# Optimization experiments

Measured on AMD Instinct MI355X. Metric: run time of the kernel, lower is better.

Reference implementation:

```python
import jax, jax.numpy as jnp
import numpy as np

B, S, D, H, L, FF = 32, 512, 256, 8, 2, 512
E = 64  # embed_dim_per_feature
VOCABS = [20, 50, 100]
NCLS = 36
MAX_CONN, THR = 10, 0.6


def _ln(x, g, b, eps=1e-5):
    m = x.mean(-1, keepdims=True)
    v = ((x - m) ** 2).mean(-1, keepdims=True)
    return g * (x - m) / jnp.sqrt(v + eps) + b


def _build_adj(cat, cnt):
    # self loops + chain links + banded similarity links (create_mutation_graph_optimized)
    Bb, _, Ss = cat.shape
    adj = jnp.broadcast_to(jnp.eye(Ss, dtype=jnp.float32), (Bb, Ss, Ss))
    for d in range(1, MAX_CONN):
        if d >= Ss:
            break
        cat_sim = (cat[:, :, :-d] == cat[:, :, d:]).astype(jnp.float32).mean(1)
        cnt_sim = jnp.exp(-jnp.abs(cnt[:, :-d] - cnt[:, d:]) / 100.0)
        sim = 0.5 * (cat_sim + cnt_sim)  # [B, S-d]
        base = 1.0 if d == 1 else 0.0  # chain link stays 1 when sim<=thr
        val = jnp.where(sim > THR, sim, base)
        ii = jnp.arange(Ss - d)
        adj = adj.at[:, ii, ii + d].set(val)
        adj = adj.at[:, ii + d, ii].set(val)
    return adj


def setup_inputs():
    key = jax.random.key(0)
    ks = iter(jax.random.split(key, 40))
    def nrm(shape, s=0.02):
        return jax.random.normal(next(ks), shape, jnp.float32) * s
    return {
        "categorical_x": jax.random.randint(next(ks), (B, 3, S), 0, min(VOCABS)),
        "count_x": jax.random.uniform(next(ks), (B, S), jnp.float32) * 100.0,
        "emb0": nrm((VOCABS[0], E)), "emb1": nrm((VOCABS[1], E)), "emb2": nrm((VOCABS[2], E)),
        "cnt_W": nrm((1, E)), "cnt_b": jnp.zeros((E,), jnp.float32),
        "pos_enc": nrm((S, D)),
        "gat_W": nrm((L, D, D)), "gat_a": nrm((L, 2 * D, 1)),
        "qkv_W": nrm((L, 3 * D, D)), "qkv_b": jnp.zeros((L, 3 * D), jnp.float32),
        "outp_W": nrm((L, D, D)), "outp_b": jnp.zeros((L, D), jnp.float32),
        "ff1_W": nrm((L, FF, D)), "ff1_b": jnp.zeros((L, FF), jnp.float32),
        "ff2_W": nrm((L, D, FF)), "ff2_b": jnp.zeros((L, D), jnp.float32),
        "ln_g": jnp.ones((L, 3, D), jnp.float32), "ln_b": jnp.zeros((L, 3, D), jnp.float32),
        "cls1_W": nrm((D // 2, D)), "cls1_b": jnp.zeros((D // 2,), jnp.float32),
        "cls2_W": nrm((NCLS, D // 2)), "cls2_b": jnp.zeros((NCLS,), jnp.float32),
    }


def reference(categorical_x, count_x, emb0, emb1, emb2, cnt_W, cnt_b, pos_enc,
              gat_W, gat_a, qkv_W, qkv_b, outp_W, outp_b,
              ff1_W, ff1_b, ff2_W, ff2_b, ln_g, ln_b,
              cls1_W, cls1_b, cls2_W, cls2_b):
    Ss = categorical_x.shape[2]
    # per-timestep feature embedding + count projection, concat -> d_model
    x = jnp.concatenate([
        emb0[categorical_x[:, 0]], emb1[categorical_x[:, 1]], emb2[categorical_x[:, 2]],
        count_x[..., None] @ cnt_W + cnt_b], -1)
    x = x + pos_enc[:Ss]
    mask = _build_adj(categorical_x, count_x) > 0  # adj used only as mask
    dh = D // H
    for l in range(L):
        # GraphAttentionLayer: e_ij = Wh_i.a1 + Wh_j.a2 (same math as repeat+concat+matmul)
        Wh = x @ gat_W[l]
        e = (Wh @ gat_a[l][:D, 0])[:, :, None] + (Wh @ gat_a[l][D:, 0])[:, None, :]
        att = jax.nn.softmax(jnp.where(mask, e, -9e15), -1)
        g = jax.nn.elu(att @ Wh)
        x = _ln(x + g, ln_g[l, 0], ln_b[l, 0])
        # MultiheadAttention (batch_first, eval)
        qkv = x @ qkv_W[l].T + qkv_b[l]
        q, k, v = jnp.split(qkv, 3, -1)
        q = q.reshape(-1, Ss, H, dh)
        k = k.reshape(-1, Ss, H, dh)
        v = v.reshape(-1, Ss, H, dh)
        sc = jnp.einsum('bihd,bjhd->bhij', q, k) / jnp.sqrt(jnp.float32(dh))
        o = jnp.einsum('bhij,bjhd->bihd', jax.nn.softmax(sc, -1), v).reshape(-1, Ss, D)
        o = o @ outp_W[l].T + outp_b[l]
        x = _ln(x + o, ln_g[l, 1], ln_b[l, 1])
        # FFN
        ff = jax.nn.relu(x @ ff1_W[l].T + ff1_b[l]) @ ff2_W[l].T + ff2_b[l]
        x = _ln(x + ff, ln_g[l, 2], ln_b[l, 2])
    pooled = x.mean(1)
    h = jax.nn.relu(pooled @ cls1_W.T + cls1_b)
    return h @ cls2_W.T + cls2_b
```

## Files before the change

### kernel.cpp

```cpp
#include <hip/hip_runtime.h>
#include <hip/hip_bf16.h>
#include <math.h>

#define Bn 32
#define Sn 512
#define Dn 256
#define Hn 8
#define DHn 32
#define En 64
#define FFn 512
#define Ln 2
#define NCLSn 36
#define BANDR 9
#define NBn 19
#define Mn (Bn * Sn)

typedef __attribute__((ext_vector_type(8))) short s8v;
typedef __attribute__((ext_vector_type(4))) float f4v;
typedef __attribute__((ext_vector_type(4))) unsigned short us4;
typedef unsigned short ushortT;

__device__ __forceinline__ ushortT f2b(float f) {
    unsigned u = __float_as_uint(f);
    unsigned r = (u + 0x7FFFu + ((u >> 16) & 1u)) >> 16;
    return (ushortT)r;
}

#define GLDS16(g, l)                                                            \
    __builtin_amdgcn_global_load_lds(                                           \
        (const __attribute__((address_space(1))) void*)(g),                     \
        (__attribute__((address_space(3))) void*)(l), 16, 0, 0)

__global__ void k_f2b(const float* __restrict__ in, ushortT* __restrict__ out, int n) {
    int i = (blockIdx.x * blockDim.x + threadIdx.x) * 4;
    if (i >= n) return;
    float4 v = *(const float4*)(in + i);
    out[i + 0] = f2b(v.x); out[i + 1] = f2b(v.y);
    out[i + 2] = f2b(v.z); out[i + 3] = f2b(v.w);
}

__global__ void k_f2bT(const float* __restrict__ in, ushortT* __restrict__ out) {
    int i = blockIdx.x * 256 + threadIdx.x;
    int l = i >> 16, rem = i & 65535;
    int k = rem >> 8, n = rem & 255;
    out[(l << 16) + n * 256 + k] = f2b(in[i]);
}

__global__ void k_embed(const int* __restrict__ cat, const float* __restrict__ cnt,
                        const float* __restrict__ e0, const float* __restrict__ e1,
                        const float* __restrict__ e2,
                        const float* __restrict__ cW, const float* __restrict__ cb,
                        const float* __restrict__ pos, float* __restrict__ x,
                        ushortT* __restrict__ xb) {
    int bs = blockIdx.x;
    int d = threadIdx.x;
    int b = bs >> 9, s = bs & 511;
    float v;
    if (d < 64)       v = e0[cat[(b * 3 + 0) * Sn + s] * En + d];
    else if (d < 128) v = e1[cat[(b * 3 + 1) * Sn + s] * En + (d - 64)];
    else if (d < 192) v = e2[cat[(b * 3 + 2) * Sn + s] * En + (d - 128)];
    else              v = cnt[b * Sn + s] * cW[d - 192] + cb[d - 192];
    float y = v + pos[s * Dn + d];
    x[(size_t)bs * Dn + d] = y;
    xb[(size_t)bs * Dn + d] = f2b(y);
}

__global__ void k_mask(const int* __restrict__ cat, const float* __restrict__ cnt,
                       unsigned char* __restrict__ mask) {
    int idx = blockIdx.x * blockDim.x + threadIdx.x;
    if (idx >= Bn * Sn * NBn) return;
    int off = idx % NBn;
    int bs = idx / NBn;
    int b = bs >> 9, i = bs & 511;
    int j = i + off - BANDR;
    unsigned char m = 0;
    if (j >= 0 && j < Sn) {
        int dd = off - BANDR;
        int ad = dd < 0 ? -dd : dd;
        if (ad <= 1) {
            m = 1;
        } else {
            int c = 0;
            for (int f = 0; f < 3; f++)
                c += (cat[(b * 3 + f) * Sn + i] == cat[(b * 3 + f) * Sn + j]);
            float cat_sim = (float)c / 3.0f;
            float cnt_sim = expf(-fabsf(cnt[b * Sn + i] - cnt[b * Sn + j]) / 100.0f);
            float sim = 0.5f * (cat_sim + cnt_sim);
            m = (sim > 0.6f) ? 1 : 0;
        }
    }
    mask[idx] = m;
}

template <int BM, int OUTBF, int ACT>
__global__ __launch_bounds__(256) void k_gemm_mfma(const ushortT* __restrict__ A,
                                                   const ushortT* __restrict__ Bt,
                                                   const float* __restrict__ bias,
                                                   void* __restrict__ Cout,
                                                   int M, int N, int K) {
    constexpr int NF = (BM == 128) ? 4 : 2;
    constexpr int CW = (BM == 128) ? 64 : 32;
    __shared__ ushortT As[BM * 32];
    __shared__ ushortT Bs[128 * 32];
    int tid = threadIdx.x;
    int w = tid >> 6, lane = tid & 63;
    int g = lane >> 4, lr = lane & 15;
    int m0 = blockIdx.y * BM, n0 = blockIdx.x * 128;
    int wr, wc;
    if constexpr (BM == 128) { wr = w >> 1; wc = w & 1; }
    else { wr = 0; wc = w; }
    f4v acc[4][NF];
#pragma unroll
    for (int m = 0; m < 4; m++)
#pragma unroll
        for (int n = 0; n < NF; n++) acc[m][n] = (f4v){0.f, 0.f, 0.f, 0.f};

    for (int k0 = 0; k0 < K; k0 += 32) {
        if constexpr (BM == 128) {
#pragma unroll
            for (int r = 0; r < 2; r++) {
                int e = (tid + r * 256) * 8;
                int row = e >> 5, kk = e & 31;
                GLDS16(A + (size_t)(m0 + row) * K + k0 + kk, As + e);
                GLDS16(Bt + (size_t)(n0 + row) * K + k0 + kk, Bs + e);
            }
        } else {
            {
                int e = tid * 8;
                int row = e >> 5, kk = e & 31;
                GLDS16(A + (size_t)(m0 + row) * K + k0 + kk, As + e);
            }
#pragma unroll
            for (int r = 0; r < 2; r++) {
                int e = (tid + r * 256) * 8;
                int row = e >> 5, kk = e & 31;
                GLDS16(Bt + (size_t)(n0 + row) * K + k0 + kk, Bs + e);
            }
        }
        __syncthreads();
        s8v af[4], bf[NF];
#pragma unroll
        for (int m = 0; m < 4; m++)
            af[m] = *(const s8v*)(As + (wr * 64 + m * 16 + lr) * 32 + g * 8);
#pragma unroll
        for (int n = 0; n < NF; n++)
            bf[n] = *(const s8v*)(Bs + (wc * CW + n * 16 + lr) * 32 + g * 8);
#pragma unroll
        for (int m = 0; m < 4; m++)
#pragma unroll
            for (int n = 0; n < NF; n++)
                acc[m][n] = __builtin_amdgcn_mfma_f32_16x16x32_bf16(af[m], bf[n], acc[m][n], 0, 0, 0);
        __syncthreads();
    }
#pragma unroll
    for (int m = 0; m < 4; m++) {
#pragma unroll
        for (int n = 0; n < NF; n++) {
            int col = n0 + wc * CW + n * 16 + lr;
            float bv = bias ? bias[col] : 0.0f;
#pragma unroll
            for (int r = 0; r < 4; r++) {
                int row = m0 + wr * 64 + m * 16 + g * 4 + r;
                float v = acc[m][n][r] + bv;
                if (ACT == 1) v = fmaxf(v, 0.0f);
                if (OUTBF)
                    ((ushortT*)Cout)[(size_t)row * N + col] = f2b(v);
                else
                    ((float*)Cout)[(size_t)row * N + col] = v;
            }
        }
    }
}

__global__ __launch_bounds__(256) void k_gat_scores(const float* __restrict__ Wh,
                                                    const float* __restrict__ ga,
                                                    float* __restrict__ a1h,
                                                    float* __restrict__ a2h) {
    int w = threadIdx.x >> 6, l = threadIdx.x & 63;
    int bs = blockIdx.x * 4 + w;
    float4 wh = *(const float4*)(Wh + (size_t)bs * Dn + l * 4);
    float4 A1 = *(const float4*)(ga + l * 4);
    float4 A2 = *(const float4*)(ga + Dn + l * 4);
    float s1 = wh.x * A1.x + wh.y * A1.y + wh.z * A1.z + wh.w * A1.w;
    float s2 = wh.x * A2.x + wh.y * A2.y + wh.z * A2.z + wh.w * A2.w;
#pragma unroll
    for (int o = 32; o; o >>= 1) {
        s1 += __shfl_xor(s1, o);
        s2 += __shfl_xor(s2, o);
    }
    if (l == 0) { a1h[bs] = s1; a2h[bs] = s2; }
}

__global__ __launch_bounds__(256) void k_gat_attn_ln(const float* __restrict__ Wh,
                                                     const float* __restrict__ a1h,
                                                     const float* __restrict__ a2h,
                                                     const unsigned char* __restrict__ mask,
                                                     const float* __restrict__ lg,
                                                     const float* __restrict__ lb,
                                                     float* __restrict__ x,
                                                     ushortT* __restrict__ xb) {
    int w = threadIdx.x >> 6, l = threadIdx.x & 63;
    int bs = blockIdx.x * 4 + w;
    int b = bs >> 9, i = bs & 511;
    float e = -1e30f;
    int j = i + l - BANDR;
    if (l < NBn && j >= 0 && j < Sn && mask[bs * NBn + l])
        e = a1h[bs] + a2h[(b << 9) + j];
    float mx = e;
#pragma unroll
    for (int o = 32; o; o >>= 1) mx = fmaxf(mx, __shfl_xor(mx, o));
    float p = (e > -1e29f) ? __expf(e - mx) : 0.0f;
    float sum = p;
#pragma unroll
    for (int o = 32; o; o >>= 1) sum += __shfl_xor(sum, o);
    p *= (1.0f / sum);
    int c4 = l * 4;
    const float* whb = Wh + (size_t)(b << 9) * Dn + c4;
    float gx = 0.f, gy = 0.f, gz = 0.f, gw = 0.f;
#pragma unroll
    for (int o = 0; o < NBn; o++) {
        float wo = __shfl(p, o);
        int jo = i + o - BANDR;
        jo = jo < 0 ? 0 : (jo > Sn - 1 ? Sn - 1 : jo);
        float4 v = *(const float4*)(whb + (size_t)jo * Dn);
        gx += wo * v.x; gy += wo * v.y; gz += wo * v.z; gw += wo * v.w;
    }
    gx = gx > 0.f ? gx : expm1f(gx);
    gy = gy > 0.f ? gy : expm1f(gy);
    gz = gz > 0.f ? gz : expm1f(gz);
    gw = gw > 0.f ? gw : expm1f(gw);
    float4 xv = *(const float4*)(x + (size_t)bs * Dn + c4);
    float y0 = xv.x + gx, y1 = xv.y + gy, y2 = xv.z + gz, y3 = xv.w + gw;
    float s1 = y0 + y1 + y2 + y3;
    float s2 = y0 * y0 + y1 * y1 + y2 * y2 + y3 * y3;
#pragma unroll
    for (int o = 32; o; o >>= 1) {
        s1 += __shfl_xor(s1, o);
        s2 += __shfl_xor(s2, o);
    }
    float mean = s1 * (1.0f / Dn);
    float var = s2 * (1.0f / Dn) - mean * mean;
    float r = rsqrtf(var + 1e-5f);
    float4 lgv = *(const float4*)(lg + c4);
    float4 lbv = *(const float4*)(lb + c4);
    float o0 = lgv.x * (y0 - mean) * r + lbv.x;
    float o1 = lgv.y * (y1 - mean) * r + lbv.y;
    float o2 = lgv.z * (y2 - mean) * r + lbv.z;
    float o3 = lgv.w * (y3 - mean) * r + lbv.w;
    *(float4*)(x + (size_t)bs * Dn + c4) = make_float4(o0, o1, o2, o3);
    us4 ob = {f2b(o0), f2b(o1), f2b(o2), f2b(o3)};
    *(us4*)(xb + (size_t)bs * Dn + c4) = ob;
}

__global__ __launch_bounds__(256) void k_attn_mfma(const ushortT* __restrict__ qkv,
                                                   ushortT* __restrict__ ob) {
    __shared__ ushortT Ks[2][64 * 32];
    __shared__ ushortT Vt[2][32 * 64];
    __shared__ ushortT Ps[4][16 * 72];
    int tid = threadIdx.x;
    int w = tid >> 6, lane = tid & 63;
    int g = lane >> 4, lr = lane & 15;
    int blk = blockIdx.x;
    int qh = blk & 1, h = (blk >> 1) & 7, b = blk >> 4;
    const ushortT* base = qkv + (size_t)b * Sn * 768;
    const ushortT* kbase = base + 256 + h * 32;
    const ushortT* vbase = base + 512 + h * 32;

    int krow2 = tid >> 3;
    int kc = (tid & 7) ^ (krow2 & 7);
    int kkv = krow2 * 2 + (kc >> 2);
    int kdd = (kc & 3) * 8;
    int vd0 = w * 8;

    int q0 = qh * 256 + w * 64;
    s8v qf[4];
#pragma unroll
    for (int m = 0; m < 4; m++)
        qf[m] = *(const s8v*)(base + (size_t)(q0 + m * 16 + lr) * 768 + h * 32 + g * 8);

    f4v o[4][2];
    float rl[4][4];
#pragma unroll
    for (int m = 0; m < 4; m++) {
        o[m][0] = (f4v){0.f, 0.f, 0.f, 0.f};
        o[m][1] = (f4v){0.f, 0.f, 0.f, 0.f};
#pragma unroll
        for (int r = 0; r < 4; r++) rl[m][r] = 0.f;
    }
    const float scale = 0.17677669529663687f;

    {
        GLDS16(kbase + (size_t)kkv * 768 + kdd, &Ks[0][tid * 8]);
        us4 v0 = *(const us4*)(vbase + (size_t)lane * 768 + vd0);
        us4 v1 = *(const us4*)(vbase + (size_t)lane * 768 + vd0 + 4);
#pragma unroll
        for (int jj = 0; jj < 4; jj++) {
            int d = vd0 + jj;
            Vt[0][d * 64 + (lane ^ ((d & 7) << 3))] = v0[jj];
            int d2 = d + 4;
            Vt[0][d2 * 64 + (lane ^ ((d2 & 7) << 3))] = v1[jj];
        }
    }
    __syncthreads();

    for (int kt = 0; kt < 8; kt++) {
        int cur = kt & 1, nxt = cur ^ 1;
        us4 v0, v1;
        if (kt < 7) {
            GLDS16(kbase + (size_t)((kt + 1) * 64 + kkv) * 768 + kdd, &Ks[nxt][tid * 8]);
            v0 = *(const us4*)(vbase + (size_t)((kt + 1) * 64 + lane) * 768 + vd0);
            v1 = *(const us4*)(vbase + (size_t)((kt + 1) * 64 + lane) * 768 + vd0 + 4);
        }
        s8v vf[2][2];
#pragma unroll
        for (int cd = 0; cd < 2; cd++)
#pragma unroll
            for (int c2 = 0; c2 < 2; c2++) {
                int d = cd * 16 + lr;
                vf[cd][c2] = *(const s8v*)(&Vt[cur][d * 64 + ((c2 * 32 + g * 8) ^ ((d & 7) << 3))]);
            }
#pragma unroll
        for (int m = 0; m < 4; m++) {
            f4v s[4];
#pragma unroll
            for (int n = 0; n < 4; n++) {
                int row2 = n * 8 + (lr >> 1);
                int cc = (((lr & 1) << 2) + g) ^ (row2 & 7);
                s8v kf = *(const s8v*)(&Ks[cur][row2 * 64 + cc * 8]);
                f4v z = (f4v){0.f, 0.f, 0.f, 0.f};
                s[n] = __builtin_amdgcn_mfma_f32_16x16x32_bf16(qf[m], kf, z, 0, 0, 0);
            }
#pragma unroll
            for (int r = 0; r < 4; r++) {
                float p0 = __expf(fminf(s[0][r] * scale, 60.f));
                float p1 = __expf(fminf(s[1][r] * scale, 60.f));
                float p2 = __expf(fminf(s[2][r] * scale, 60.f));
                float p3 = __expf(fminf(s[3][r] * scale, 60.f));
                rl[m][r] += (p0 + p1) + (p2 + p3);
                int rr = g * 4 + r;
                Ps[w][rr * 72 + lr]      = f2b(p0);
                Ps[w][rr * 72 + 16 + lr] = f2b(p1);
                Ps[w][rr * 72 + 32 + lr] = f2b(p2);
                Ps[w][rr * 72 + 48 + lr] = f2b(p3);
            }
            s8v pf0 = *(const s8v*)(&Ps[w][lr * 72 + g * 8]);
            s8v pf1 = *(const s8v*)(&Ps[w][lr * 72 + 32 + g * 8]);
            o[m][0] = __builtin_amdgcn_mfma_f32_16x16x32_bf16(pf0, vf[0][0], o[m][0], 0, 0, 0);
            o[m][0] = __builtin_amdgcn_mfma_f32_16x16x32_bf16(pf1, vf[0][1], o[m][0], 0, 0, 0);
            o[m][1] = __builtin_amdgcn_mfma_f32_16x16x32_bf16(pf0, vf[1][0], o[m][1], 0, 0, 0);
            o[m][1] = __builtin_amdgcn_mfma_f32_16x16x32_bf16(pf1, vf[1][1], o[m][1], 0, 0, 0);
        }
        if (kt < 7) {
#pragma unroll
            for (int jj = 0; jj < 4; jj++) {
                int d = vd0 + jj;
                Vt[nxt][d * 64 + (lane ^ ((d & 7) << 3))] = v0[jj];
                int d2 = d + 4;
                Vt[nxt][d2 * 64 + (lane ^ ((d2 & 7) << 3))] = v1[jj];
            }
        }
        __syncthreads();
    }
#pragma unroll
    for (int m = 0; m < 4; m++) {
#pragma unroll
        for (int r = 0; r < 4; r++) {
            float t = rl[m][r];
            t += __shfl_xor(t, 1);
            t += __shfl_xor(t, 2);
            t += __shfl_xor(t, 4);
            t += __shfl_xor(t, 8);
            float inv = 1.0f / t;
            int qr = q0 + m * 16 + g * 4 + r;
            size_t obase = ((size_t)(b * Sn + qr)) * Dn + h * 32;
            ob[obase + lr] = f2b(o[m][0][r] * inv);
            ob[obase + 16 + lr] = f2b(o[m][1][r] * inv);
        }
    }
}

__global__ __launch_bounds__(256) void k_ln_add(float* __restrict__ x, const float* __restrict__ t,
                                                const float* __restrict__ lg, const float* __restrict__ lb,
                                                ushortT* __restrict__ xb) {
    int w = threadIdx.x >> 6, l = threadIdx.x & 63;
    int bs = blockIdx.x * 4 + w;
    int c4 = l * 4;
    float4 xv = *(const float4*)(x + (size_t)bs * Dn + c4);
    float4 tv = *(const float4*)(t + (size_t)bs * Dn + c4);
    float y0 = xv.x + tv.x, y1 = xv.y + tv.y, y2 = xv.z + tv.z, y3 = xv.w + tv.w;
    float s1 = y0 + y1 + y2 + y3;
    float s2 = y0 * y0 + y1 * y1 + y2 * y2 + y3 * y3;
#pragma unroll
    for (int o = 32; o; o >>= 1) {
        s1 += __shfl_xor(s1, o);
        s2 += __shfl_xor(s2, o);
    }
    float mean = s1 * (1.0f / Dn);
    float var = s2 * (1.0f / Dn) - mean * mean;
    float r = rsqrtf(var + 1e-5f);
    float4 lgv = *(const float4*)(lg + c4);
    float4 lbv = *(const float4*)(lb + c4);
    float o0 = lgv.x * (y0 - mean) * r + lbv.x;
    float o1 = lgv.y * (y1 - mean) * r + lbv.y;
    float o2 = lgv.z * (y2 - mean) * r + lbv.z;
    float o3 = lgv.w * (y3 - mean) * r + lbv.w;
    *(float4*)(x + (size_t)bs * Dn + c4) = make_float4(o0, o1, o2, o3);
    us4 ob = {f2b(o0), f2b(o1), f2b(o2), f2b(o3)};
    *(us4*)(xb + (size_t)bs * Dn + c4) = ob;
}

__global__ void k_pool(const float* __restrict__ x, float* __restrict__ part) {
    int b = blockIdx.x, sc = blockIdx.y;
    int t = threadIdx.x;
    float s = 0.f;
    for (int s0 = 0; s0 < 64; s0++)
        s += x[((size_t)(b << 9) + sc * 64 + s0) * Dn + t];
    part[(b * 8 + sc) * Dn + t] = s;
}

__global__ void k_cls(const float* __restrict__ part, const float* __restrict__ w1,
                      const float* __restrict__ b1, const float* __restrict__ w2,
                      const float* __restrict__ b2, float* __restrict__ out) {
    int b = blockIdx.x;
    int t = threadIdx.x;
    __shared__ float pooled[Dn];
    __shared__ float hbuf[128];
    float s = 0.f;
#pragma unroll
    for (int k = 0; k < 8; k++) s += part[(b * 8 + k) * Dn + t];
    pooled[t] = s * (1.0f / Sn);
    __syncthreads();
    if (t < 128) {
        float a = b1[t];
        for (int k = 0; k < Dn; k++) a += pooled[k] * w1[t * Dn + k];
        hbuf[t] = fmaxf(a, 0.0f);
    }
    __syncthreads();
    if (t < NCLSn) {
        float a2 = b2[t];
        for (int k = 0; k < 128; k++) a2 += hbuf[k] * w2[t * 128 + k];
        out[b * NCLSn + t] = a2;
    }
}

extern "C" void kernel_launch(void* const* d_in, const int* in_sizes, int n_in,
                              void* d_out, int out_size, void* d_ws, size_t ws_size,
                              hipStream_t stream) {
    const int* cat = (const int*)d_in[0];
    const float* cnt = (const float*)d_in[1];
    const float* emb0 = (const float*)d_in[2];
    const float* emb1 = (const float*)d_in[3];
    const float* emb2 = (const float*)d_in[4];
    const float* cnt_W = (const float*)d_in[5];
    const float* cnt_b = (const float*)d_in[6];
    const float* pos_enc = (const float*)d_in[7];
    const float* gat_W = (const float*)d_in[8];
    const float* gat_a = (const float*)d_in[9];
    const float* qkv_W = (const float*)d_in[10];
    const float* qkv_b = (const float*)d_in[11];
    const float* outp_W = (const float*)d_in[12];
    const float* outp_b = (const float*)d_in[13];
    const float* ff1_W = (const float*)d_in[14];
    const float* ff1_b = (const float*)d_in[15];
    const float* ff2_W = (const float*)d_in[16];
    const float* ff2_b = (const float*)d_in[17];
    const float* ln_g = (const float*)d_in[18];
    const float* ln_b = (const float*)d_in[19];
    const float* cls1_W = (const float*)d_in[20];
    const float* cls1_b = (const float*)d_in[21];
    const float* cls2_W = (const float*)d_in[22];
    const float* cls2_b = (const float*)d_in[23];
    float* out = (float*)d_out;

    char* wp = (char*)d_ws;
    float* x = (float*)wp;        wp += (size_t)Mn * Dn * 4;
    float* tmpf = (float*)wp;     wp += (size_t)Mn * Dn * 4;
    ushortT* xb = (ushortT*)wp;   wp += (size_t)Mn * Dn * 2;
    ushortT* qkvb = (ushortT*)wp; wp += (size_t)Mn * 3 * Dn * 2;
    ushortT* ffb = qkvb;
    ushortT* obb = (ushortT*)wp;  wp += (size_t)Mn * Dn * 2;
    float* a1h = (float*)wp;      wp += (size_t)Mn * 4;
    float* a2h = (float*)wp;      wp += (size_t)Mn * 4;
    float* part = (float*)wp;     wp += (size_t)Bn * 8 * Dn * 4;
    unsigned char* mask = (unsigned char*)wp; wp += (size_t)Mn * NBn;
    ushortT* gatWb = (ushortT*)wp;  wp += (size_t)Ln * Dn * Dn * 2;
    ushortT* qkvWb = (ushortT*)wp;  wp += (size_t)Ln * 3 * Dn * Dn * 2;
    ushortT* outpWb = (ushortT*)wp; wp += (size_t)Ln * Dn * Dn * 2;
    ushortT* ff1Wb = (ushortT*)wp;  wp += (size_t)Ln * FFn * Dn * 2;
    ushortT* ff2Wb = (ushortT*)wp;  wp += (size_t)Ln * Dn * FFn * 2;

    k_f2bT<<<Ln * 65536 / 256, 256, 0, stream>>>(gat_W, gatWb);
    k_f2b<<<(Ln * 3 * Dn * Dn / 4 + 255) / 256, 256, 0, stream>>>(qkv_W, qkvWb, Ln * 3 * Dn * Dn);
    k_f2b<<<(Ln * Dn * Dn / 4 + 255) / 256, 256, 0, stream>>>(outp_W, outpWb, Ln * Dn * Dn);
    k_f2b<<<(Ln * FFn * Dn / 4 + 255) / 256, 256, 0, stream>>>(ff1_W, ff1Wb, Ln * FFn * Dn);
    k_f2b<<<(Ln * Dn * FFn / 4 + 255) / 256, 256, 0, stream>>>(ff2_W, ff2Wb, Ln * Dn * FFn);

    k_embed<<<Mn, Dn, 0, stream>>>(cat, cnt, emb0, emb1, emb2, cnt_W, cnt_b, pos_enc, x, xb);
    k_mask<<<(Bn * Sn * NBn + 255) / 256, 256, 0, stream>>>(cat, cnt, mask);

    for (int l = 0; l < Ln; l++) {
        k_gemm_mfma<64, 0, 0><<<dim3(Dn / 128, Mn / 64), 256, 0, stream>>>(
            xb, gatWb + (size_t)l * Dn * Dn, nullptr, tmpf, Mn, Dn, Dn);
        k_gat_scores<<<Mn / 4, 256, 0, stream>>>(tmpf, gat_a + (size_t)l * 2 * Dn, a1h, a2h);
        k_gat_attn_ln<<<Mn / 4, 256, 0, stream>>>(tmpf, a1h, a2h, mask,
                                                  ln_g + (l * 3 + 0) * Dn, ln_b + (l * 3 + 0) * Dn, x, xb);
        k_gemm_mfma<128, 1, 0><<<dim3(3 * Dn / 128, Mn / 128), 256, 0, stream>>>(
            xb, qkvWb + (size_t)l * 3 * Dn * Dn, qkv_b + l * 3 * Dn, qkvb, Mn, 3 * Dn, Dn);
        k_attn_mfma<<<Bn * Hn * 2, 256, 0, stream>>>(qkvb, obb);
        k_gemm_mfma<64, 0, 0><<<dim3(Dn / 128, Mn / 64), 256, 0, stream>>>(
            obb, outpWb + (size_t)l * Dn * Dn, outp_b + l * Dn, tmpf, Mn, Dn, Dn);
        k_ln_add<<<Mn / 4, 256, 0, stream>>>(x, tmpf, ln_g + (l * 3 + 1) * Dn, ln_b + (l * 3 + 1) * Dn, xb);
        k_gemm_mfma<128, 1, 1><<<dim3(FFn / 128, Mn / 128), 256, 0, stream>>>(
            xb, ff1Wb + (size_t)l * FFn * Dn, ff1_b + l * FFn, ffb, Mn, FFn, Dn);
        k_gemm_mfma<64, 0, 0><<<dim3(Dn / 128, Mn / 64), 256, 0, stream>>>(
            ffb, ff2Wb + (size_t)l * Dn * FFn, ff2_b + l * Dn, tmpf, Mn, Dn, FFn);
        k_ln_add<<<Mn / 4, 256, 0, stream>>>(x, tmpf, ln_g + (l * 3 + 2) * Dn, ln_b + (l * 3 + 2) * Dn, xb);
    }

    k_pool<<<dim3(Bn, 8), 256, 0, stream>>>(x, part);
    k_cls<<<Bn, Dn, 0, stream>>>(part, cls1_W, cls1_b, cls2_W, cls2_b, out);
}
```

Before: 350.4 us.

## Fuse GAT scores and residual LayerNorm into full-row GEMM epilogues with double buffering

Adds a full-row GEMM kernel with 64-row tiles covering all 256 columns. One variant computes the GAT attention score projections in the epilogue, and the other adds bias and the residual and then applies LayerNorm. This removes the separate gat_scores and ln_add kernels and the fp32 round trip of intermediate outputs through global memory. The square-tile GEMM now double-buffers its LDS tiles so the next tile load overlaps the MFMAs. The attention kernel hoists K fragment loads out of the m loop. The tradeoff is fewer blocks (256) for the row-GEMM launches and higher LDS use.

```diff
diff --git a/kernel.cpp b/kernel.cpp
--- a/kernel.cpp
+++ b/kernel.cpp
@@ -92,103 +92,211 @@
     mask[idx] = m;
 }
 
-template <int BM, int OUTBF, int ACT>
+template <int ACT>
 __global__ __launch_bounds__(256) void k_gemm_mfma(const ushortT* __restrict__ A,
                                                    const ushortT* __restrict__ Bt,
                                                    const float* __restrict__ bias,
-                                                   void* __restrict__ Cout,
+                                                   ushortT* __restrict__ Cout,
                                                    int M, int N, int K) {
-    constexpr int NF = (BM == 128) ? 4 : 2;
-    constexpr int CW = (BM == 128) ? 64 : 32;
-    __shared__ ushortT As[BM * 32];
-    __shared__ ushortT Bs[128 * 32];
+    __shared__ ushortT As[2][128 * 32];
+    __shared__ ushortT Bs[2][128 * 32];
     int tid = threadIdx.x;
     int w = tid >> 6, lane = tid & 63;
     int g = lane >> 4, lr = lane & 15;
-    int m0 = blockIdx.y * BM, n0 = blockIdx.x * 128;
-    int wr, wc;
-    if constexpr (BM == 128) { wr = w >> 1; wc = w & 1; }
-    else { wr = 0; wc = w; }
-    f4v acc[4][NF];
+    int m0 = blockIdx.y * 128, n0 = blockIdx.x * 128;
+    int wr = w >> 1, wc = w & 1;
+    int NT = K >> 5;
+    f4v acc[4][4];
 #pragma unroll
     for (int m = 0; m < 4; m++)
 #pragma unroll
-        for (int n = 0; n < NF; n++) acc[m][n] = (f4v){0.f, 0.f, 0.f, 0.f};
-
-    for (int k0 = 0; k0 < K; k0 += 32) {
-        if constexpr (BM == 128) {
-#pragma unroll
-            for (int r = 0; r < 2; r++) {
-                int e = (tid + r * 256) * 8;
-                int row = e >> 5, kk = e & 31;
-                GLDS16(A + (size_t)(m0 + row) * K + k0 + kk, As + e);
-                GLDS16(Bt + (size_t)(n0 + row) * K + k0 + kk, Bs + e);
-            }
-        } else {
-            {
-                int e = tid * 8;
-                int row = e >> 5, kk = e & 31;
-                GLDS16(A + (size_t)(m0 + row) * K + k0 + kk, As + e);
-            }
-#pragma unroll
-            for (int r = 0; r < 2; r++) {
-                int e = (tid + r * 256) * 8;
-                int row = e >> 5, kk = e & 31;
-                GLDS16(Bt + (size_t)(n0 + row) * K + k0 + kk, Bs + e);
-            }
-        }
-        __syncthreads();
-        s8v af[4], bf[NF];
+        for (int n = 0; n < 4; n++) acc[m][n] = (f4v){0.f, 0.f, 0.f, 0.f};
+
+    auto stage = [&](int t, int buf) {
+        int k0 = t << 5;
+#pragma unroll
+        for (int r = 0; r < 2; r++) {
+            int e = (tid + r * 256) * 8;
+            int row = e >> 5, kk = e & 31;
+            GLDS16(A + (size_t)(m0 + row) * K + k0 + kk, &As[buf][e]);
+            GLDS16(Bt + (size_t)(n0 + row) * K + k0 + kk, &Bs[buf][e]);
+        }
+    };
+
+    stage(0, 0);
+    __syncthreads();
+    for (int t = 0; t < NT; t++) {
+        int cur = t & 1;
+        if (t + 1 < NT) stage(t + 1, cur ^ 1);
+        s8v af[4], bf[4];
 #pragma unroll
         for (int m = 0; m < 4; m++)
-            af[m] = *(const s8v*)(As + (wr * 64 + m * 16 + lr) * 32 + g * 8);
-#pragma unroll
-        for (int n = 0; n < NF; n++)
-            bf[n] = *(const s8v*)(Bs + (wc * CW + n * 16 + lr) * 32 + g * 8);
+            af[m] = *(const s8v*)(&As[cur][(wr * 64 + m * 16 + lr) * 32 + g * 8]);
+#pragma unroll
+        for (int n = 0; n < 4; n++)
+            bf[n] = *(const s8v*)(&Bs[cur][(wc * 64 + n * 16 + lr) * 32 + g * 8]);
 #pragma unroll
         for (int m = 0; m < 4; m++)
 #pragma unroll
-            for (int n = 0; n < NF; n++)
+            for (int n = 0; n < 4; n++)
                 acc[m][n] = __builtin_amdgcn_mfma_f32_16x16x32_bf16(af[m], bf[n], acc[m][n], 0, 0, 0);
         __syncthreads();
     }
 #pragma unroll
     for (int m = 0; m < 4; m++) {
 #pragma unroll
-        for (int n = 0; n < NF; n++) {
-            int col = n0 + wc * CW + n * 16 + lr;
+        for (int n = 0; n < 4; n++) {
+            int col = n0 + wc * 64 + n * 16 + lr;
             float bv = bias ? bias[col] : 0.0f;
 #pragma unroll
             for (int r = 0; r < 4; r++) {
                 int row = m0 + wr * 64 + m * 16 + g * 4 + r;
                 float v = acc[m][n][r] + bv;
                 if (ACT == 1) v = fmaxf(v, 0.0f);
-                if (OUTBF)
-                    ((ushortT*)Cout)[(size_t)row * N + col] = f2b(v);
-                else
-                    ((float*)Cout)[(size_t)row * N + col] = v;
-            }
-        }
-    }
-}
-
-__global__ __launch_bounds__(256) void k_gat_scores(const float* __restrict__ Wh,
-                                                    const float* __restrict__ ga,
-                                                    float* __restrict__ a1h,
-                                                    float* __restrict__ a2h) {
-    int w = threadIdx.x >> 6, l = threadIdx.x & 63;
-    int bs = blockIdx.x * 4 + w;
-    float4 wh = *(const float4*)(Wh + (size_t)bs * Dn + l * 4);
-    float4 A1 = *(const float4*)(ga + l * 4);
-    float4 A2 = *(const float4*)(ga + Dn + l * 4);
-    float s1 = wh.x * A1.x + wh.y * A1.y + wh.z * A1.z + wh.w * A1.w;
-    float s2 = wh.x * A2.x + wh.y * A2.y + wh.z * A2.z + wh.w * A2.w;
-#pragma unroll
-    for (int o = 32; o; o >>= 1) {
-        s1 += __shfl_xor(s1, o);
-        s2 += __shfl_xor(s2, o);
-    }
-    if (l == 0) { a1h[bs] = s1; a2h[bs] = s2; }
+                Cout[(size_t)row * N + col] = f2b(v);
+            }
+        }
+    }
+}
+
+template <int MODE>
+__global__ __launch_bounds__(512) void k_gemm_row(const ushortT* __restrict__ A,
+                                                  const ushortT* __restrict__ Bt,
+                                                  const float* __restrict__ bias,
+                                                  const float* __restrict__ ga,
+                                                  float* __restrict__ a1h, float* __restrict__ a2h,
+                                                  float* __restrict__ Whout,
+                                                  const float* __restrict__ lg,
+                                                  const float* __restrict__ lb,
+                                                  float* __restrict__ x, ushortT* __restrict__ xb,
+                                                  int K) {
+    __shared__ ushortT As[2][64 * 32];
+    __shared__ ushortT Bs[2][256 * 32];
+    __shared__ float red1[64][4], red2[64][4];
+    int tid = threadIdx.x;
+    int w = tid >> 6, lane = tid & 63;
+    int g = lane >> 4, lr = lane & 15;
+    int wr = w >> 2, wc = w & 3;
+    int m0 = blockIdx.x * 64;
+    int NT = K >> 5;
+    f4v acc[2][4];
+#pragma unroll
+    for (int m = 0; m < 2; m++)
+#pragma unroll
+        for (int n = 0; n < 4; n++) acc[m][n] = (f4v){0.f, 0.f, 0.f, 0.f};
+
+    auto stage = [&](int t, int buf) {
+        int k0 = t << 5;
+        if (tid < 256) {
+            int e = tid * 8;
+            int row = e >> 5, kk = e & 31;
+            GLDS16(A + (size_t)(m0 + row) * K + k0 + kk, &As[buf][e]);
+        }
+#pragma unroll
+        for (int r = 0; r < 2; r++) {
+            int e = (tid + r * 512) * 8;
+            int row = e >> 5, kk = e & 31;
+            GLDS16(Bt + (size_t)row * K + k0 + kk, &Bs[buf][e]);
+        }
+    };
+
+    stage(0, 0);
+    __syncthreads();
+    for (int t = 0; t < NT; t++) {
+        int cur = t & 1;
+        if (t + 1 < NT) stage(t + 1, cur ^ 1);
+        s8v af[2], bf[4];
+#pragma unroll
+        for (int m = 0; m < 2; m++)
+            af[m] = *(const s8v*)(&As[cur][(wr * 32 + m * 16 + lr) * 32 + g * 8]);
+#pragma unroll
+        for (int n = 0; n < 4; n++)
+            bf[n] = *(const s8v*)(&Bs[cur][(wc * 64 + n * 16 + lr) * 32 + g * 8]);
+#pragma unroll
+        for (int m = 0; m < 2; m++)
+#pragma unroll
+            for (int n = 0; n < 4; n++)
+                acc[m][n] = __builtin_amdgcn_mfma_f32_16x16x32_bf16(af[m], bf[n], acc[m][n], 0, 0, 0);
+        __syncthreads();
+    }
+
+    int cn[4];
+#pragma unroll
+    for (int n = 0; n < 4; n++) cn[n] = wc * 64 + n * 16 + lr;
+
+    if constexpr (MODE == 0) {
+        float a1v[4], a2v[4];
+#pragma unroll
+        for (int n = 0; n < 4; n++) { a1v[n] = ga[cn[n]]; a2v[n] = ga[Dn + cn[n]]; }
+#pragma unroll
+        for (int m = 0; m < 2; m++)
+#pragma unroll
+            for (int r = 0; r < 4; r++) {
+                int rowl = wr * 32 + m * 16 + g * 4 + r;
+                float p1 = 0.f, p2 = 0.f;
+#pragma unroll
+                for (int n = 0; n < 4; n++) {
+                    float v = acc[m][n][r];
+                    Whout[(size_t)(m0 + rowl) * Dn + cn[n]] = v;
+                    p1 += v * a1v[n];
+                    p2 += v * a2v[n];
+                }
+                p1 += __shfl_xor(p1, 1); p2 += __shfl_xor(p2, 1);
+                p1 += __shfl_xor(p1, 2); p2 += __shfl_xor(p2, 2);
+                p1 += __shfl_xor(p1, 4); p2 += __shfl_xor(p2, 4);
+                p1 += __shfl_xor(p1, 8); p2 += __shfl_xor(p2, 8);
+                if (lr == 0) { red1[rowl][wc] = p1; red2[rowl][wc] = p2; }
+            }
+        __syncthreads();
+        if (tid < 64) {
+            float t1 = red1[tid][0] + red1[tid][1] + red1[tid][2] + red1[tid][3];
+            float t2 = red2[tid][0] + red2[tid][1] + red2[tid][2] + red2[tid][3];
+            a1h[m0 + tid] = t1;
+            a2h[m0 + tid] = t2;
+        }
+    } else {
+        float bv[4], lgv[4], lbv[4];
+#pragma unroll
+        for (int n = 0; n < 4; n++) { bv[n] = bias[cn[n]]; lgv[n] = lg[cn[n]]; lbv[n] = lb[cn[n]]; }
+#pragma unroll
+        for (int m = 0; m < 2; m++)
+#pragma unroll
+            for (int r = 0; r < 4; r++) {
+                int rowl = wr * 32 + m * 16 + g * 4 + r;
+                float s1 = 0.f, s2 = 0.f;
+#pragma unroll
+                for (int n = 0; n < 4; n++) {
+                    float y = acc[m][n][r] + bv[n] + x[(size_t)(m0 + rowl) * Dn + cn[n]];
+                    acc[m][n][r] = y;
+                    s1 += y;
+                    s2 += y * y;
+                }
+                s1 += __shfl_xor(s1, 1); s2 += __shfl_xor(s2, 1);
+                s1 += __shfl_xor(s1, 2); s2 += __shfl_xor(s2, 2);
+                s1 += __shfl_xor(s1, 4); s2 += __shfl_xor(s2, 4);
+                s1 += __shfl_xor(s1, 8); s2 += __shfl_xor(s2, 8);
+                if (lr == 0) { red1[rowl][wc] = s1; red2[rowl][wc] = s2; }
+            }
+        __syncthreads();
+#pragma unroll
+        for (int m = 0; m < 2; m++)
+#pragma unroll
+            for (int r = 0; r < 4; r++) {
+                int rowl = wr * 32 + m * 16 + g * 4 + r;
+                float S1 = red1[rowl][0] + red1[rowl][1] + red1[rowl][2] + red1[rowl][3];
+                float S2 = red2[rowl][0] + red2[rowl][1] + red2[rowl][2] + red2[rowl][3];
+                float mean = S1 * (1.0f / Dn);
+                float var = S2 * (1.0f / Dn) - mean * mean;
+                float rs = rsqrtf(var + 1e-5f);
+#pragma unroll
+                for (int n = 0; n < 4; n++) {
+                    float o = lgv[n] * (acc[m][n][r] - mean) * rs + lbv[n];
+                    size_t idx = (size_t)(m0 + rowl) * Dn + cn[n];
+                    x[idx] = o;
+                    xb[idx] = f2b(o);
+                }
+            }
+    }
 }
 
 __global__ __launch_bounds__(256) void k_gat_attn_ln(const float* __restrict__ Wh,
@@ -311,6 +419,13 @@
             v0 = *(const us4*)(vbase + (size_t)((kt + 1) * 64 + lane) * 768 + vd0);
             v1 = *(const us4*)(vbase + (size_t)((kt + 1) * 64 + lane) * 768 + vd0 + 4);
         }
+        s8v kf[4];
+#pragma unroll
+        for (int n = 0; n < 4; n++) {
+            int row2 = n * 8 + (lr >> 1);
+            int cc = (((lr & 1) << 2) + g) ^ (row2 & 7);
+            kf[n] = *(const s8v*)(&Ks[cur][row2 * 64 + cc * 8]);
+        }
         s8v vf[2][2];
 #pragma unroll
         for (int cd = 0; cd < 2; cd++)
@@ -324,11 +439,8 @@
             f4v s[4];
 #pragma unroll
             for (int n = 0; n < 4; n++) {
-                int row2 = n * 8 + (lr >> 1);
-                int cc = (((lr & 1) << 2) + g) ^ (row2 & 7);
-                s8v kf = *(const s8v*)(&Ks[cur][row2 * 64 + cc * 8]);
                 f4v z = (f4v){0.f, 0.f, 0.f, 0.f};
-                s[n] = __builtin_amdgcn_mfma_f32_16x16x32_bf16(qf[m], kf, z, 0, 0, 0);
+                s[n] = __builtin_amdgcn_mfma_f32_16x16x32_bf16(qf[m], kf[n], z, 0, 0, 0);
             }
 #pragma unroll
             for (int r = 0; r < 4; r++) {
@@ -377,36 +489,6 @@
             ob[obase + 16 + lr] = f2b(o[m][1][r] * inv);
         }
     }
-}
-
-__global__ __launch_bounds__(256) void k_ln_add(float* __restrict__ x, const float* __restrict__ t,
-                                                const float* __restrict__ lg, const float* __restrict__ lb,
-                                                ushortT* __restrict__ xb) {
-    int w = threadIdx.x >> 6, l = threadIdx.x & 63;
-    int bs = blockIdx.x * 4 + w;
-    int c4 = l * 4;
-    float4 xv = *(const float4*)(x + (size_t)bs * Dn + c4);
-    float4 tv = *(const float4*)(t + (size_t)bs * Dn + c4);
-    float y0 = xv.x + tv.x, y1 = xv.y + tv.y, y2 = xv.z + tv.z, y3 = xv.w + tv.w;
-    float s1 = y0 + y1 + y2 + y3;
-    float s2 = y0 * y0 + y1 * y1 + y2 * y2 + y3 * y3;
-#pragma unroll
-    for (int o = 32; o; o >>= 1) {
-        s1 += __shfl_xor(s1, o);
-        s2 += __shfl_xor(s2, o);
-    }
-    float mean = s1 * (1.0f / Dn);
-    float var = s2 * (1.0f / Dn) - mean * mean;
-    float r = rsqrtf(var + 1e-5f);
-    float4 lgv = *(const float4*)(lg + c4);
-    float4 lbv = *(const float4*)(lb + c4);
-    float o0 = lgv.x * (y0 - mean) * r + lbv.x;
-    float o1 = lgv.y * (y1 - mean) * r + lbv.y;
-    float o2 = lgv.z * (y2 - mean) * r + lbv.z;
-    float o3 = lgv.w * (y3 - mean) * r + lbv.w;
-    *(float4*)(x + (size_t)bs * Dn + c4) = make_float4(o0, o1, o2, o3);
-    us4 ob = {f2b(o0), f2b(o1), f2b(o2), f2b(o3)};
-    *(us4*)(xb + (size_t)bs * Dn + c4) = ob;
 }
 
 __global__ void k_pool(const float* __restrict__ x, float* __restrict__ part) {
@@ -499,22 +581,25 @@
     k_mask<<<(Bn * Sn * NBn + 255) / 256, 256, 0, stream>>>(cat, cnt, mask);
 
     for (int l = 0; l < Ln; l++) {
-        k_gemm_mfma<64, 0, 0><<<dim3(Dn / 128, Mn / 64), 256, 0, stream>>>(
-            xb, gatWb + (size_t)l * Dn * Dn, nullptr, tmpf, Mn, Dn, Dn);
-        k_gat_scores<<<Mn / 4, 256, 0, stream>>>(tmpf, gat_a + (size_t)l * 2 * Dn, a1h, a2h);
+        k_gemm_row<0><<<Mn / 64, 512, 0, stream>>>(
+            xb, gatWb + (size_t)l * Dn * Dn, nullptr,
+            gat_a + (size_t)l * 2 * Dn, a1h, a2h, tmpf,
+            nullptr, nullptr, nullptr, nullptr, Dn);
         k_gat_attn_ln<<<Mn / 4, 256, 0, stream>>>(tmpf, a1h, a2h, mask,
                                                   ln_g + (l * 3 + 0) * Dn, ln_b + (l * 3 + 0) * Dn, x, xb);
-        k_gemm_mfma<128, 1, 0><<<dim3(3 * Dn / 128, Mn / 128), 256, 0, stream>>>(
+        k_gemm_mfma<0><<<dim3(3 * Dn / 128, Mn / 128), 256, 0, stream>>>(
             xb, qkvWb + (size_t)l * 3 * Dn * Dn, qkv_b + l * 3 * Dn, qkvb, Mn, 3 * Dn, Dn);
         k_attn_mfma<<<Bn * Hn * 2, 256, 0, stream>>>(qkvb, obb);
-        k_gemm_mfma<64, 0, 0><<<dim3(Dn / 128, Mn / 64), 256, 0, stream>>>(
-            obb, outpWb + (size_t)l * Dn * Dn, outp_b + l * Dn, tmpf, Mn, Dn, Dn);
-        k_ln_add<<<Mn / 4, 256, 0, stream>>>(x, tmpf, ln_g + (l * 3 + 1) * Dn, ln_b + (l * 3 + 1) * Dn, xb);
-        k_gemm_mfma<128, 1, 1><<<dim3(FFn / 128, Mn / 128), 256, 0, stream>>>(
+        k_gemm_row<1><<<Mn / 64, 512, 0, stream>>>(
+            obb, outpWb + (size_t)l * Dn * Dn, outp_b + l * Dn,
+            nullptr, nullptr, nullptr, nullptr,
+            ln_g + (l * 3 + 1) * Dn, ln_b + (l * 3 + 1) * Dn, x, xb, Dn);
+        k_gemm_mfma<1><<<dim3(FFn / 128, Mn / 128), 256, 0, stream>>>(
             xb, ff1Wb + (size_t)l * FFn * Dn, ff1_b + l * FFn, ffb, Mn, FFn, Dn);
-        k_gemm_mfma<64, 0, 0><<<dim3(Dn / 128, Mn / 64), 256, 0, stream>>>(
-            ffb, ff2Wb + (size_t)l * Dn * FFn, ff2_b + l * Dn, tmpf, Mn, Dn, FFn);
-        k_ln_add<<<Mn / 4, 256, 0, stream>>>(x, tmpf, ln_g + (l * 3 + 2) * Dn, ln_b + (l * 3 + 2) * Dn, xb);
+        k_gemm_row<1><<<Mn / 64, 512, 0, stream>>>(
+            ffb, ff2Wb + (size_t)l * Dn * FFn, ff2_b + l * Dn,
+            nullptr, nullptr, nullptr, nullptr,
+            ln_g + (l * 3 + 2) * Dn, ln_b + (l * 3 + 2) * Dn, x, xb, FFn);
     }
 
     k_pool<<<dim3(Bn, 8), 256, 0, stream>>>(x, part);
```

Result: faster. 317.6 us (-9.4%).
